# Kernel tuning notes

Hardware: AMD Instinct MI355X
Metric: run time of the kernel (lower is better)

## Reference

```python
import jax, jax.numpy as jnp
import numpy as np

B, S, D, H, W = 2, 2048, 1024, 16, 128
HD = D // H
EPS = 1e-5
NEG = -1e9


def setup_inputs() -> dict:
    key = jax.random.key(0)
    ks = jax.random.split(key, 6)
    sd = 1.0 / np.sqrt(D)
    return {
        "x": jax.random.normal(ks[0], (B, S, D), jnp.float32),
        "Wq": jax.random.normal(ks[1], (D, D), jnp.float32) * sd,
        "bq": jnp.zeros((D,), jnp.float32),
        "Wk": jax.random.normal(ks[2], (D, D), jnp.float32) * sd,
        "bk": jnp.zeros((D,), jnp.float32),
        "Wv": jax.random.normal(ks[3], (D, D), jnp.float32) * sd,
        "bv": jnp.zeros((D,), jnp.float32),
        "Wo": jax.random.normal(ks[4], (D, D), jnp.float32) * sd,
        "bo": jnp.zeros((D,), jnp.float32),
        "gamma": jnp.ones((D,), jnp.float32),
        "beta": jnp.zeros((D,), jnp.float32),
    }


def _local_causal_mask(seq_len, window):
    pos = jnp.arange(seq_len)
    qp = pos[:, None]
    kp = pos[None, :]
    return (jnp.abs(qp - kp) < window) & (qp >= kp)  # [S, S] bool


def reference(x, Wq, bq, Wk, bk, Wv, bv, Wo, bo, gamma, beta):
    scale = 1.0 / np.sqrt(HD)
    # projections -> [B, H, S, HD]
    def split_heads(t):
        return t.reshape(B, S, H, HD).transpose(0, 2, 1, 3)

    q = split_heads(x @ Wq + bq)
    k = split_heads(x @ Wk + bk)
    v = split_heads(x @ Wv + bv)

    scores = jnp.einsum("bhqd,bhkd->bhqk", q, k) * scale  # [B,H,S,S]
    mask = _local_causal_mask(S, W)
    scores = jnp.where(mask[None, None, :, :], scores, NEG)
    attn = jax.nn.softmax(scores, axis=-1)
    out = jnp.einsum("bhqk,bhkd->bhqd", attn, v)  # [B,H,S,HD]
    out = out.transpose(0, 2, 1, 3).reshape(B, S, D)
    out = out @ Wo + bo

    # residual + LayerNorm(eps=1e-5)
    y = x + out
    mu = jnp.mean(y, axis=-1, keepdims=True)
    var = jnp.mean(jnp.square(y - mu), axis=-1, keepdims=True)
    y = (y - mu) * jax.lax.rsqrt(var + EPS) * gamma + beta
    return y
```

## Files before the change

kernel.cpp:

```cpp
#include <hip/hip_runtime.h>
#include <hip/hip_bf16.h>

typedef __hip_bfloat16 bf16;
typedef float f32x4 __attribute__((ext_vector_type(4)));
typedef short bf16x8 __attribute__((ext_vector_type(8)));
typedef int   int4v  __attribute__((ext_vector_type(4)));

constexpr int Bb = 2, Ss = 2048, Dd = 1024, Hh = 16, Ww = 128, HDd = 64;
constexpr int Mrows = Bb * Ss;
constexpr int NTk = Dd / 64;

__device__ __forceinline__ void gload16(const void* g, void* l) {
  __builtin_amdgcn_global_load_lds(
      (const __attribute__((address_space(1))) void*)g,
      (__attribute__((address_space(3))) void*)l, 16, 0, 0);
}

__device__ __forceinline__ f32x4 mfma16(bf16x8 a, bf16x8 b, f32x4 c) {
  return __builtin_amdgcn_mfma_f32_16x16x32_bf16(a, b, c, 0, 0, 0);
}

__global__ __launch_bounds__(256) void prep_k(const float* __restrict__ x,
                                              const float* __restrict__ W0,
                                              const float* __restrict__ W1,
                                              const float* __restrict__ W2,
                                              const float* __restrict__ W3,
                                              bf16* __restrict__ xb,
                                              bf16* __restrict__ Wt) {
  if (blockIdx.z == 4) {
    size_t blk = blockIdx.y * 32 + blockIdx.x;
#pragma unroll
    for (int it = 0; it < 4; ++it) {
      size_t i = blk * 1024 + it * 256 + threadIdx.x;
      float4 v = reinterpret_cast<const float4*>(x)[i];
      union { bf16 b[4]; ushort4 u; } cv;
      cv.b[0] = __float2bfloat16(v.x);
      cv.b[1] = __float2bfloat16(v.y);
      cv.b[2] = __float2bfloat16(v.z);
      cv.b[3] = __float2bfloat16(v.w);
      reinterpret_cast<ushort4*>(xb)[i] = cv.u;
    }
    return;
  }
  const float* Win = (blockIdx.z == 0) ? W0 : (blockIdx.z == 1) ? W1
                     : (blockIdx.z == 2) ? W2 : W3;
  bf16* o = Wt + (size_t)blockIdx.z * Dd * Dd;
  __shared__ float tile[32][33];
  int bx = blockIdx.x, by = blockIdx.y;
  int tx = threadIdx.x & 31, ty = threadIdx.x >> 5;
#pragma unroll
  for (int i = 0; i < 4; ++i)
    tile[ty + i * 8][tx] = Win[(size_t)(by * 32 + ty + i * 8) * Dd + bx * 32 + tx];
  __syncthreads();
#pragma unroll
  for (int i = 0; i < 4; ++i)
    o[(size_t)(bx * 32 + ty + i * 8) * Dd + by * 32 + tx] =
        __float2bfloat16(tile[tx][ty + i * 8]);
}

__device__ __forceinline__ void gemm_core8(const bf16* __restrict__ A,
                                           const bf16* __restrict__ Bt,
                                           int bm, int bn,
                                           bf16* lds, f32x4 acc[2][4]) {
  const int t = threadIdx.x;
  const int lane = t & 63, w = t >> 6;
  const int wr = w >> 1, wc = w & 1;
  const int l15 = lane & 15, l16 = lane >> 4;
  const bf16* Arow0 = A + (size_t)bm * 128 * Dd;
  const bf16* Brow0 = Bt + (size_t)bn * 128 * Dd;

  auto stage = [&](int buf, int kt) {
#pragma unroll
    for (int i = 0; i < 2; ++i) {
      int ci = i * 512 + t;
      int row = ci >> 3, pc = ci & 7;
      int sc = pc ^ (row & 7);
      gload16(Arow0 + (size_t)row * Dd + kt * 64 + sc * 8, lds + buf * 16384 + ci * 8);
      gload16(Brow0 + (size_t)row * Dd + kt * 64 + sc * 8, lds + buf * 16384 + 8192 + ci * 8);
    }
  };

  stage(0, 0);
  __syncthreads();
  int buf = 0;
  for (int kt = 0; kt < NTk; ++kt) {
    if (kt + 1 < NTk) stage(buf ^ 1, kt + 1);
    bf16x8 af[2][2], bfr[4][2];
    const bf16* Ab = lds + buf * 16384;
    const bf16* Bb = Ab + 8192;
#pragma unroll
    for (int m = 0; m < 2; ++m) {
      int row = wr * 32 + m * 16 + l15;
#pragma unroll
      for (int kk = 0; kk < 2; ++kk)
        af[m][kk] = *reinterpret_cast<const bf16x8*>(
            Ab + row * 64 + (((kk * 4 + l16) ^ (row & 7)) * 8));
    }
#pragma unroll
    for (int n = 0; n < 4; ++n) {
      int row = wc * 64 + n * 16 + l15;
#pragma unroll
      for (int kk = 0; kk < 2; ++kk)
        bfr[n][kk] = *reinterpret_cast<const bf16x8*>(
            Bb + row * 64 + (((kk * 4 + l16) ^ (row & 7)) * 8));
    }
    __builtin_amdgcn_s_setprio(1);
#pragma unroll
    for (int m = 0; m < 2; ++m)
#pragma unroll
      for (int n = 0; n < 4; ++n) {
        acc[m][n] = mfma16(af[m][0], bfr[n][0], acc[m][n]);
        acc[m][n] = mfma16(af[m][1], bfr[n][1], acc[m][n]);
      }
    __builtin_amdgcn_s_setprio(0);
    __syncthreads();
    buf ^= 1;
  }
}

__global__ __launch_bounds__(512) void gemm_qkv8w(const bf16* __restrict__ A,
                                                  const bf16* __restrict__ Wt3,
                                                  const float* __restrict__ bq,
                                                  const float* __restrict__ bk,
                                                  const float* __restrict__ bv,
                                                  bf16* __restrict__ Qh,
                                                  bf16* __restrict__ Kh,
                                                  bf16* __restrict__ Vt) {
  __shared__ __align__(16) bf16 lds[32768];
  f32x4 acc[2][4] = {};
  int id = blockIdx.x;
  int xcd = id & 7, j = id >> 3;
  int sb = j / 24, rem = j % 24;
  int bm = xcd * 4 + rem / 6;
  int bn = sb * 6 + rem % 6;
  gemm_core8(A, Wt3, bm, bn, lds, acc);

  const int lane = threadIdx.x & 63, w = threadIdx.x >> 6;
  const int wr = w >> 1, wc = w & 1, l15 = lane & 15, l16 = lane >> 4;
  const int p = bn >> 3;
  const int c0w = (bn & 7) * 128 + wc * 64;
  const int h = c0w >> 6;

  if (p < 2) {
    bf16 (*rep)[72] = reinterpret_cast<bf16(*)[72]>(lds + w * (16 * 72));
    bf16* dst = p ? Kh : Qh;
    const float* bp = p ? bk : bq;
    float bi[4];
#pragma unroll
    for (int n = 0; n < 4; ++n) bi[n] = bp[c0w + n * 16 + l15];
#pragma unroll
    for (int m = 0; m < 2; ++m) {
#pragma unroll
      for (int n = 0; n < 4; ++n)
#pragma unroll
        for (int r = 0; r < 4; ++r)
          rep[l16 * 4 + r][n * 16 + l15] = __float2bfloat16(acc[m][n][r] + bi[n]);
      int rrow = lane >> 2, rch = lane & 3;
      int sg = bm * 128 + wr * 32 + m * 16 + rrow;
      int b = sg >> 11, sl = sg & (Ss - 1);
      bf16* base = dst + (((size_t)(b * Hh + h)) * Ss + sl) * HDd;
      bf16x8 v0 = *reinterpret_cast<const bf16x8*>(&rep[rrow][rch * 8]);
      bf16x8 v1 = *reinterpret_cast<const bf16x8*>(&rep[rrow][(rch + 4) * 8]);
      *reinterpret_cast<bf16x8*>(base + rch * 8) = v0;
      *reinterpret_cast<bf16x8*>(base + (rch + 4) * 8) = v1;
    }
  } else {
#pragma unroll
    for (int n = 0; n < 4; ++n) {
      int col = c0w + n * 16 + l15;
      int hh = col >> 6, hd = col & (HDd - 1);
      float bi = bv[col];
#pragma unroll
      for (int m = 0; m < 2; ++m) {
        int s0 = bm * 128 + wr * 32 + m * 16 + l16 * 4;
        int b = s0 >> 11, sl = s0 & (Ss - 1);
        union { ushort4 u; ushort e[4]; } pk;
#pragma unroll
        for (int r = 0; r < 4; ++r) {
          bf16 tb = __float2bfloat16(acc[m][n][r] + bi);
          pk.e[r] = *reinterpret_cast<ushort*>(&tb);
        }
        *reinterpret_cast<ushort4*>(&Vt[(((size_t)(b * Hh + hh)) * HDd + hd) * Ss + sl]) = pk.u;
      }
    }
  }
}

__global__ __launch_bounds__(512) void gemm_o8w(const bf16* __restrict__ AO,
                                                const bf16* __restrict__ WtO,
                                                const float* __restrict__ bo,
                                                const float* __restrict__ resid,
                                                float* __restrict__ out) {
  __shared__ __align__(16) bf16 lds[32768];
  f32x4 acc[2][4] = {};
  int id = blockIdx.x;
  int wg = (id & 7) * 32 + (id >> 3);
  int bm = wg >> 3, bn = wg & 7;
  gemm_core8(AO, WtO, bm, bn, lds, acc);

  const int lane = threadIdx.x & 63, w = threadIdx.x >> 6;
  const int wr = w >> 1, wc = w & 1, l15 = lane & 15, l16 = lane >> 4;
#pragma unroll
  for (int m = 0; m < 2; ++m)
#pragma unroll
    for (int n = 0; n < 4; ++n) {
      int col = bn * 128 + wc * 64 + n * 16 + l15;
      float bi = bo[col];
#pragma unroll
      for (int r = 0; r < 4; ++r) {
        int row = bm * 128 + wr * 32 + m * 16 + l16 * 4 + r;
        size_t idx = (size_t)row * Dd + col;
        out[idx] = acc[m][n][r] + bi + resid[idx];
      }
    }
}

__global__ __launch_bounds__(512) void attn_local2(const bf16* __restrict__ Q,
                                                   const bf16* __restrict__ K,
                                                   const bf16* __restrict__ Vt,
                                                   bf16* __restrict__ AO) {
  __shared__ __align__(16) bf16 Kl[256 * 64];
  __shared__ bf16 Ps[8][16][168];
  const int t = threadIdx.x, lane = t & 63, w = t >> 6;
  const int l15 = lane & 15, l16 = lane >> 4;
  const int qb = blockIdx.x, h = blockIdx.y, b = blockIdx.z;
  const int q0 = qb * 128, kstart = q0 - 128;
  const bf16* Qp = Q + ((size_t)(b * Hh + h)) * Ss * HDd;
  const bf16* Kp = K + ((size_t)(b * Hh + h)) * Ss * HDd;
  const bf16* Vp = Vt + ((size_t)(b * Hh + h)) * HDd * Ss;

#pragma unroll
  for (int i = 0; i < 4; ++i) {
    int ci = i * 512 + t;
    int row = ci >> 3, pc = ci & 7;
    int sc = pc ^ (row & 7);
    int key = kstart + row;
    if (key < 0) key = 0;
    gload16(Kp + (size_t)key * HDd + sc * 8, (bf16*)Kl + ci * 8);
  }

  const int qrow = q0 + w * 16 + l15;
  bf16x8 aq0 = *reinterpret_cast<const bf16x8*>(Qp + (size_t)qrow * HDd + l16 * 8);
  bf16x8 aq1 = *reinterpret_cast<const bf16x8*>(Qp + (size_t)qrow * HDd + 32 + l16 * 8);

  __syncthreads();

  f32x4 sc9[9];
  __builtin_amdgcn_s_setprio(1);
#pragma unroll
  for (int j = 0; j < 9; ++j) {
    int krow = (w + j) * 16 + l15;
    bf16x8 bk0 = *reinterpret_cast<const bf16x8*>(
        Kl + krow * 64 + (((0 + l16) ^ (krow & 7)) * 8));
    bf16x8 bk1 = *reinterpret_cast<const bf16x8*>(
        Kl + krow * 64 + (((4 + l16) ^ (krow & 7)) * 8));
    f32x4 s = {};
    s = mfma16(aq0, bk0, s);
    s = mfma16(aq1, bk1, s);
    sc9[j] = s;
  }
  __builtin_amdgcn_s_setprio(0);

  const float scale = 0.125f;
  float mrow[4], ssum[4], inv[4];
  int qg[4];
#pragma unroll
  for (int r = 0; r < 4; ++r) { mrow[r] = -1e30f; qg[r] = q0 + w * 16 + l16 * 4 + r; }
#pragma unroll
  for (int j = 0; j < 9; ++j) {
    int kg = kstart + (w + j) * 16 + l15;
#pragma unroll
    for (int r = 0; r < 4; ++r) {
      bool valid = (kg >= 0) && (kg <= qg[r]) && (qg[r] - kg < Ww);
      float v = valid ? sc9[j][r] * scale : -1e9f;
      sc9[j][r] = v;
      mrow[r] = fmaxf(mrow[r], v);
    }
  }
#pragma unroll
  for (int r = 0; r < 4; ++r)
#pragma unroll
    for (int off = 1; off < 16; off <<= 1)
      mrow[r] = fmaxf(mrow[r], __shfl_xor(mrow[r], off));
#pragma unroll
  for (int r = 0; r < 4; ++r) ssum[r] = 0.f;
#pragma unroll
  for (int j = 0; j < 9; ++j)
#pragma unroll
    for (int r = 0; r < 4; ++r) {
      float p = __expf(sc9[j][r] - mrow[r]);
      sc9[j][r] = p;
      ssum[r] += p;
    }
#pragma unroll
  for (int r = 0; r < 4; ++r)
#pragma unroll
    for (int off = 1; off < 16; off <<= 1)
      ssum[r] += __shfl_xor(ssum[r], off);
#pragma unroll
  for (int r = 0; r < 4; ++r) inv[r] = 1.f / ssum[r];

#pragma unroll
  for (int j = 0; j < 9; ++j) {
    int lt = j + (w & 1);
#pragma unroll
    for (int r = 0; r < 4; ++r)
      Ps[w][l16 * 4 + r][lt * 16 + l15] = __float2bfloat16(sc9[j][r]);
  }
  {
    int ltz = (w & 1) ? 0 : 9;
    bf16 z16 = __float2bfloat16(0.f);
#pragma unroll
    for (int r = 0; r < 4; ++r)
      Ps[w][l16 * 4 + r][ltz * 16 + l15] = z16;
  }

  f32x4 o[4] = {};
  __builtin_amdgcn_s_setprio(1);
#pragma unroll
  for (int cc = 0; cc < 5; ++cc) {
    bf16x8 pf = *reinterpret_cast<const bf16x8*>(&Ps[w][l15][cc * 32 + l16 * 8]);
    int kk = kstart + ((w >> 1) + cc) * 32 + l16 * 8;
    int kc = kk < 0 ? 0 : kk;
#pragma unroll
    for (int ht = 0; ht < 4; ++ht) {
      bf16x8 vf = *reinterpret_cast<const bf16x8*>(Vp + (size_t)(ht * 16 + l15) * Ss + kc);
      o[ht] = mfma16(pf, vf, o[ht]);
    }
  }
  __builtin_amdgcn_s_setprio(0);

#pragma unroll
  for (int ht = 0; ht < 4; ++ht)
#pragma unroll
    for (int r = 0; r < 4; ++r) {
      int qw = q0 + w * 16 + l16 * 4 + r;
      int col = h * HDd + ht * 16 + l15;
      AO[(size_t)(b * Ss + qw) * Dd + col] = __float2bfloat16(o[ht][r] * inv[r]);
    }
}

__global__ __launch_bounds__(256) void ln_inplace(float* __restrict__ y,
                                                  const float* __restrict__ gamma,
                                                  const float* __restrict__ beta) {
  int row = blockIdx.x;
  float* yr = y + (size_t)row * Dd;
  float4 v = reinterpret_cast<const float4*>(yr)[threadIdx.x];
  float s = v.x + v.y + v.z + v.w;
  float s2 = v.x * v.x + v.y * v.y + v.z * v.z + v.w * v.w;
#pragma unroll
  for (int off = 1; off < 64; off <<= 1) {
    s += __shfl_xor(s, off);
    s2 += __shfl_xor(s2, off);
  }
  __shared__ float r1[4], r2[4];
  int w = threadIdx.x >> 6;
  if ((threadIdx.x & 63) == 0) { r1[w] = s; r2[w] = s2; }
  __syncthreads();
  s = r1[0] + r1[1] + r1[2] + r1[3];
  s2 = r2[0] + r2[1] + r2[2] + r2[3];
  float mu = s * (1.f / Dd);
  float var = s2 * (1.f / Dd) - mu * mu;
  float rs = rsqrtf(var + 1e-5f);
  float4 g = reinterpret_cast<const float4*>(gamma)[threadIdx.x];
  float4 be = reinterpret_cast<const float4*>(beta)[threadIdx.x];
  float4 o;
  o.x = (v.x - mu) * rs * g.x + be.x;
  o.y = (v.y - mu) * rs * g.y + be.y;
  o.z = (v.z - mu) * rs * g.z + be.z;
  o.w = (v.w - mu) * rs * g.w + be.w;
  reinterpret_cast<float4*>(yr)[threadIdx.x] = o;
}

extern "C" void kernel_launch(void* const* d_in, const int* in_sizes, int n_in,
                              void* d_out, int out_size, void* d_ws, size_t ws_size,
                              hipStream_t stream) {
  const float* x     = (const float*)d_in[0];
  const float* Wq    = (const float*)d_in[1];
  const float* bq    = (const float*)d_in[2];
  const float* Wk    = (const float*)d_in[3];
  const float* bk    = (const float*)d_in[4];
  const float* Wv    = (const float*)d_in[5];
  const float* bv    = (const float*)d_in[6];
  const float* Wo    = (const float*)d_in[7];
  const float* bo    = (const float*)d_in[8];
  const float* gamma = (const float*)d_in[9];
  const float* beta  = (const float*)d_in[10];
  float* out = (float*)d_out;

  char* ws = (char*)d_ws;
  bf16* xb  = (bf16*)(ws + (size_t)0);
  bf16* Wt3 = (bf16*)(ws + ((size_t)8  << 20));
  bf16* WtO = (bf16*)(ws + ((size_t)14 << 20));
  bf16* Qh  = (bf16*)(ws + ((size_t)16 << 20));
  bf16* Kh  = (bf16*)(ws + ((size_t)24 << 20));
  bf16* Vt  = (bf16*)(ws + ((size_t)32 << 20));
  bf16* AO  = (bf16*)(ws + ((size_t)40 << 20));

  prep_k<<<dim3(32, 32, 5), 256, 0, stream>>>(x, Wq, Wk, Wv, Wo, xb, Wt3);

  gemm_qkv8w<<<768, 512, 0, stream>>>(xb, Wt3, bq, bk, bv, Qh, Kh, Vt);

  attn_local2<<<dim3(Ss / 128, Hh, Bb), 512, 0, stream>>>(Qh, Kh, Vt, AO);

  gemm_o8w<<<256, 512, 0, stream>>>(AO, WtO, bo, x, out);
  ln_inplace<<<Mrows, 256, 0, stream>>>(out, gamma, beta);
}
```

Before: 86.25 us.

## Deepen GEMM pipeline to four-stage K=32 ring with explicit vmcnt waits

Switches the shared GEMM core from a double-buffered K=64 tile to a four-slot ring of K=32 tiles, keeping three loads in flight. It uses explicit s_waitcnt vmcnt counts and raw barriers instead of __syncthreads, with a new XOR swizzle for 32-wide rows. The goal is to hide global-to-LDS latency better and cut full-drain syncs. The cost is twice as many barriers per K, and the hand-counted vmcnt values must match the outstanding loads exactly.

```diff
diff --git a/kernel.cpp b/kernel.cpp
--- a/kernel.cpp
+++ b/kernel.cpp
@@ -8,7 +8,7 @@
 
 constexpr int Bb = 2, Ss = 2048, Dd = 1024, Hh = 16, Ww = 128, HDd = 64;
 constexpr int Mrows = Bb * Ss;
-constexpr int NTk = Dd / 64;
+constexpr int NT32 = Dd / 32;
 
 __device__ __forceinline__ void gload16(const void* g, void* l) {
   __builtin_amdgcn_global_load_lds(
@@ -70,51 +70,47 @@
   const bf16* Brow0 = Bt + (size_t)bn * 128 * Dd;
 
   auto stage = [&](int buf, int kt) {
-#pragma unroll
-    for (int i = 0; i < 2; ++i) {
-      int ci = i * 512 + t;
-      int row = ci >> 3, pc = ci & 7;
-      int sc = pc ^ (row & 7);
-      gload16(Arow0 + (size_t)row * Dd + kt * 64 + sc * 8, lds + buf * 16384 + ci * 8);
-      gload16(Brow0 + (size_t)row * Dd + kt * 64 + sc * 8, lds + buf * 16384 + 8192 + ci * 8);
-    }
+    int ci = t;
+    int row = ci >> 2, pc = ci & 3;
+    int sc = pc ^ ((row ^ (row >> 2)) & 3);
+    gload16(Arow0 + (size_t)row * Dd + kt * 32 + sc * 8, lds + buf * 8192 + ci * 8);
+    gload16(Brow0 + (size_t)row * Dd + kt * 32 + sc * 8, lds + buf * 8192 + 4096 + ci * 8);
   };
 
-  stage(0, 0);
-  __syncthreads();
-  int buf = 0;
-  for (int kt = 0; kt < NTk; ++kt) {
-    if (kt + 1 < NTk) stage(buf ^ 1, kt + 1);
-    bf16x8 af[2][2], bfr[4][2];
-    const bf16* Ab = lds + buf * 16384;
-    const bf16* Bb = Ab + 8192;
+  stage(0, 0); stage(1, 1); stage(2, 2);
+  asm volatile("s_waitcnt vmcnt(4)" ::: "memory");
+  __builtin_amdgcn_s_barrier();
+  __builtin_amdgcn_sched_barrier(0);
+
+  for (int kt = 0; kt < NT32; ++kt) {
+    if (kt + 3 < NT32) stage((kt + 3) & 3, kt + 3);
+    const bf16* Ab = lds + (kt & 3) * 8192;
+    const bf16* Bb = Ab + 4096;
+    bf16x8 af[2], bfr[4];
 #pragma unroll
     for (int m = 0; m < 2; ++m) {
       int row = wr * 32 + m * 16 + l15;
-#pragma unroll
-      for (int kk = 0; kk < 2; ++kk)
-        af[m][kk] = *reinterpret_cast<const bf16x8*>(
-            Ab + row * 64 + (((kk * 4 + l16) ^ (row & 7)) * 8));
+      int mc = (row ^ (row >> 2)) & 3;
+      af[m] = *reinterpret_cast<const bf16x8*>(Ab + row * 32 + ((l16 ^ mc) * 8));
     }
 #pragma unroll
     for (int n = 0; n < 4; ++n) {
       int row = wc * 64 + n * 16 + l15;
-#pragma unroll
-      for (int kk = 0; kk < 2; ++kk)
-        bfr[n][kk] = *reinterpret_cast<const bf16x8*>(
-            Bb + row * 64 + (((kk * 4 + l16) ^ (row & 7)) * 8));
+      int mc = (row ^ (row >> 2)) & 3;
+      bfr[n] = *reinterpret_cast<const bf16x8*>(Bb + row * 32 + ((l16 ^ mc) * 8));
     }
     __builtin_amdgcn_s_setprio(1);
 #pragma unroll
     for (int m = 0; m < 2; ++m)
 #pragma unroll
-      for (int n = 0; n < 4; ++n) {
-        acc[m][n] = mfma16(af[m][0], bfr[n][0], acc[m][n]);
-        acc[m][n] = mfma16(af[m][1], bfr[n][1], acc[m][n]);
-      }
+      for (int n = 0; n < 4; ++n)
+        acc[m][n] = mfma16(af[m], bfr[n], acc[m][n]);
     __builtin_amdgcn_s_setprio(0);
-    __syncthreads();
-    buf ^= 1;
+    if (kt + 3 < NT32)      asm volatile("s_waitcnt vmcnt(4)" ::: "memory");
+    else if (kt + 2 < NT32) asm volatile("s_waitcnt vmcnt(2)" ::: "memory");
+    else                    asm volatile("s_waitcnt vmcnt(0)" ::: "memory");
+    __builtin_amdgcn_s_barrier();
+    __builtin_amdgcn_sched_barrier(0);
   }
 }
 
```

After: 93.09 us. +7.9%, slower.
